# Kernel tuning notes

Hardware: AMD Instinct MI355X
Metric: run time of the kernel (lower is better)

Reference implementation:

```python
import jax, jax.numpy as jnp
import numpy as np

N_NODES = 100000
N_EDGES = 1600000
VOCAB = 10000
HIDDEN = 128
EMB1 = 128
EMB2 = 128
L1 = 64
N_GRAPHS = 256


def setup_inputs() -> dict:
    key = jax.random.key(0)
    ks = jax.random.split(key, 16)
    inp = {
        "x": jax.random.randint(ks[0], (N_NODES,), 0, VOCAB, dtype=jnp.int32),
        "edge_index": jax.random.randint(ks[1], (2, N_EDGES), 0, N_NODES, dtype=jnp.int32),
        "edge_weight": jax.random.uniform(ks[2], (N_EDGES,), dtype=jnp.float32),
        "batch": jnp.sort(jax.random.randint(ks[3], (N_NODES,), 0, N_GRAPHS, dtype=jnp.int32)),
        # parameters
        "emb_w": jax.random.normal(ks[4], (VOCAB, HIDDEN), dtype=jnp.float32) * 0.5,
        "w1_rel": jax.random.normal(ks[5], (EMB1, HIDDEN), dtype=jnp.float32) * (HIDDEN ** -0.5),
        "b1_rel": jnp.zeros((EMB1,), dtype=jnp.float32),
        "w1_root": jax.random.normal(ks[6], (EMB1, HIDDEN), dtype=jnp.float32) * (HIDDEN ** -0.5),
        "w2_rel": jax.random.normal(ks[7], (EMB2, EMB1), dtype=jnp.float32) * (EMB1 ** -0.5),
        "b2_rel": jnp.zeros((EMB2,), dtype=jnp.float32),
        "w2_root": jax.random.normal(ks[8], (EMB2, EMB1), dtype=jnp.float32) * (EMB1 ** -0.5),
        "cls1_w": jax.random.normal(ks[9], (L1, EMB2), dtype=jnp.float32) * (EMB2 ** -0.5),
        "cls1_b": jnp.zeros((L1,), dtype=jnp.float32),
        "cls2_w": jax.random.normal(ks[10], (2, L1), dtype=jnp.float32) * (L1 ** -0.5),
        "cls2_b": jnp.zeros((2,), dtype=jnp.float32),
    }
    return inp


def _embedding_max_norm(emb_w, idx, max_norm=1.0):
    # torch Embedding(max_norm=1): looked-up rows are renormalized to norm <= 1
    rows = emb_w[idx]                                        # [N, H]
    norm = jnp.linalg.norm(rows, axis=-1, keepdims=True)
    scale = jnp.minimum(1.0, max_norm / (norm + 1e-7))
    return rows * scale


def _graph_conv(h, src, dst, ew, w_rel, b_rel, w_root):
    # PyG GraphConv: out = lin_rel(sum_{j->i} w_ji * x_j) + lin_root(x_i)
    msg = h[src] * ew[:, None]                               # [E, D] gather
    agg = jax.ops.segment_sum(msg, dst, num_segments=N_NODES)  # [N, D] scatter-add
    return agg @ w_rel.T + b_rel + h @ w_root.T


def reference(x, edge_index, edge_weight, batch, emb_w,
              w1_rel, b1_rel, w1_root, w2_rel, b2_rel, w2_root,
              cls1_w, cls1_b, cls2_w, cls2_b):
    src, dst = edge_index[0], edge_index[1]
    h = _embedding_max_norm(emb_w, x)                        # [N, HIDDEN]
    # dropout is identity in eval mode
    h = jax.nn.relu(_graph_conv(h, src, dst, edge_weight, w1_rel, b1_rel, w1_root))
    h = jax.nn.relu(_graph_conv(h, src, dst, edge_weight, w2_rel, b2_rel, w2_root))
    # global mean pool over graphs
    sums = jax.ops.segment_sum(h, batch, num_segments=N_GRAPHS)        # [G, EMB2]
    counts = jax.ops.segment_sum(jnp.ones((h.shape[0],), h.dtype), batch,
                                 num_segments=N_GRAPHS)
    pooled = sums / jnp.maximum(counts, 1.0)[:, None]
    z = jax.nn.relu(pooled @ cls1_w.T + cls1_b)
    z = z @ cls2_w.T + cls2_b
    return jax.nn.softmax(z, axis=1)                          # [G, 2]
```

## Files before the change

### kernel.cpp

```cpp
#include <hip/hip_runtime.h>
#include <stdint.h>

#define NN 100000
#define NE 1600000
#define NG 256
#define NB 391
#define CHUNK 4096
#define NCH 391
#define NGS 392

typedef __attribute__((ext_vector_type(8))) short bf16x8;
typedef __attribute__((ext_vector_type(4))) float f32x4;

__device__ inline uint32_t f2bf(float f){
    uint32_t u = __float_as_uint(f);
    return (u + 0x7FFFu + ((u >> 16) & 1u)) >> 16;
}
__device__ inline float bflo(uint32_t u){ return __uint_as_float(u << 16); }
__device__ inline float bfhi(uint32_t u){ return __uint_as_float(u & 0xFFFF0000u); }
__device__ inline float bf1(short s){ return __uint_as_float(((uint32_t)(uint16_t)s) << 16); }

__global__ __launch_bounds__(256) void k_pack(const float* __restrict__ w1rel, const float* __restrict__ w1root,
                                              const float* __restrict__ w2rel, const float* __restrict__ w2root,
                                              short* __restrict__ wf, int* __restrict__ bcnt){
    int id = blockIdx.x * 256 + threadIdx.x;
    if (id < NB) bcnt[id] = 0;
    int i = id & 7, lane = (id >> 3) & 63, ks = (id >> 9) & 3, j0 = (id >> 11) & 7, m = id >> 14;
    const float* W = (m == 0) ? w1rel : (m == 1) ? w1root : (m == 2) ? w2rel : w2root;
    int j = j0 * 16 + (lane & 15);
    int k = ks * 32 + (lane >> 4) * 8 + i;
    wf[id] = (short)f2bf(W[j * 128 + k]);
}

__global__ __launch_bounds__(256) void k_embed(const int* __restrict__ x,
                                               const float* __restrict__ emb,
                                               uint32_t* __restrict__ hout,
                                               const int* __restrict__ edst,
                                               int* __restrict__ bcnt,
                                               const int* __restrict__ batch,
                                               int* __restrict__ gstart){
    int bid = blockIdx.x;
    if (bid < NN / 4){
        int w = threadIdx.x >> 6, l = threadIdx.x & 63;
        int n = bid * 4 + w;
        int r = x[n];
        const float2* e2 = (const float2*)emb;
        float2 v = e2[(size_t)r * 64 + l];
        float ss = v.x * v.x + v.y * v.y;
        #pragma unroll
        for (int off = 32; off; off >>= 1) ss += __shfl_xor(ss, off, 64);
        float sc = fminf(1.f, 1.f / (sqrtf(ss) + 1e-7f));
        hout[(size_t)n * 64 + l] = f2bf(v.x * sc) | (f2bf(v.y * sc) << 16);
    } else if (bid < NN / 4 + NCH){
        __shared__ int lh[NB];
        int t = threadIdx.x;
        int c0 = (bid - NN / 4) * CHUNK;
        int cnt = min(CHUNK, NE - c0);
        lh[t] = 0;
        if (t + 256 < NB) lh[t + 256] = 0;
        __syncthreads();
        for (int i = t; i < cnt; i += 256) atomicAdd(&lh[edst[c0 + i] >> 8], 1);
        __syncthreads();
        if (lh[t]) atomicAdd(&bcnt[t], lh[t]);
        if (t + 256 < NB && lh[t + 256]) atomicAdd(&bcnt[t + 256], lh[t + 256]);
    } else {
        int i = (bid - NN / 4 - NCH) * 256 + threadIdx.x;
        if (i > NN) return;
        int bprev = (i == 0) ? -1 : batch[i - 1];
        int bcur  = (i == NN) ? NG : batch[i];
        for (int g = bprev + 1; g <= bcur; ++g) gstart[g] = i;
    }
}

__global__ __launch_bounds__(256) void k_bscan(const int* __restrict__ bcnt,
                                               int* __restrict__ bbase, int* __restrict__ bfill,
                                               int* __restrict__ ptrA){
    __shared__ int sc[512];
    int t = threadIdx.x;
    int v0 = (t < NB) ? bcnt[t] : 0;
    int v1 = (t + 256 < NB) ? bcnt[t + 256] : 0;
    sc[t] = v0; sc[t + 256] = v1;
    __syncthreads();
    for (int off = 1; off < 512; off <<= 1){
        int u0 = (t >= off) ? sc[t - off] : 0;
        int u1 = sc[t + 256 - off];
        __syncthreads();
        sc[t] += u0; sc[t + 256] += u1;
        __syncthreads();
    }
    if (t < NB){ bbase[t] = sc[t] - v0; bfill[t] = 0; }
    if (t + 256 < NB){ bbase[t + 256] = sc[t + 256] - v1; bfill[t + 256] = 0; }
    if (t == 0){ bbase[NB] = NE; ptrA[NN] = NE; }
}

__global__ __launch_bounds__(256) void k_bscatter(const int* __restrict__ esrc, const int* __restrict__ edst,
                                                  const float* __restrict__ ew,
                                                  const int* __restrict__ bbase, int* __restrict__ bfill,
                                                  uint2* __restrict__ cse2){
    __shared__ uint2 rec[CHUNK];
    __shared__ unsigned short slotb[CHUNK];
    __shared__ int hist[512], start[512], gbase[512], sc[512];
    int t = threadIdx.x;
    int c0 = blockIdx.x * CHUNK;
    int cnt = min(CHUNK, NE - c0);
    hist[t] = 0; hist[t + 256] = 0;
    __syncthreads();
    for (int i = t; i < cnt; i += 256) atomicAdd(&hist[edst[c0 + i] >> 8], 1);
    __syncthreads();
    int v0 = hist[t], v1 = hist[t + 256];
    sc[t] = v0; sc[t + 256] = v1;
    __syncthreads();
    for (int off = 1; off < 512; off <<= 1){
        int u0 = (t >= off) ? sc[t - off] : 0;
        int u1 = sc[t + 256 - off];
        __syncthreads();
        sc[t] += u0; sc[t + 256] += u1;
        __syncthreads();
    }
    start[t] = sc[t] - v0;
    start[t + 256] = sc[t + 256] - v1;
    if (t < NB && v0 > 0) gbase[t] = bbase[t] + atomicAdd(&bfill[t], v0);
    if (t + 256 < NB && v1 > 0) gbase[t + 256] = bbase[t + 256] + atomicAdd(&bfill[t + 256], v1);
    __syncthreads();
    hist[t] = 0; hist[t + 256] = 0;
    __syncthreads();
    for (int i = t; i < cnt; i += 256){
        int d = edst[c0 + i];
        int b = d >> 8;
        int slot = start[b] + atomicAdd(&hist[b], 1);
        rec[slot] = make_uint2((uint32_t)esrc[c0 + i] | ((uint32_t)(d & 255) << 20),
                               __float_as_uint(ew[c0 + i]));
        slotb[slot] = (unsigned short)b;
    }
    __syncthreads();
    for (int i = t; i < cnt; i += 256){
        int b = slotb[i];
        cse2[gbase[b] + (i - start[b])] = rec[i];
    }
}

__global__ __launch_bounds__(256) void k_bcsr(const uint2* __restrict__ cse2,
                                              const int* __restrict__ bbase,
                                              int* __restrict__ ptrA,
                                              uint2* __restrict__ cse){
    __shared__ int cnt[256], sc[256], st[256];
    int t = threadIdx.x;
    int b = blockIdx.x;
    int ebase = bbase[b], eend = bbase[b + 1];
    int nb = b << 8;
    cnt[t] = 0;
    __syncthreads();
    for (int i = ebase + t; i < eend; i += 256){
        atomicAdd(&cnt[cse2[i].x >> 20], 1);
    }
    __syncthreads();
    int v = cnt[t];
    sc[t] = v;
    __syncthreads();
    for (int off = 1; off < 256; off <<= 1){
        int u = (t >= off) ? sc[t - off] : 0;
        __syncthreads();
        sc[t] += u;
        __syncthreads();
    }
    st[t] = sc[t] - v;
    if (nb + t < NN) ptrA[nb + t] = ebase + st[t];
    cnt[t] = 0;
    __syncthreads();
    for (int i = ebase + t; i < eend; i += 256){
        uint2 r = cse2[i];
        int dr = r.x >> 20;
        int pos = st[dr] + atomicAdd(&cnt[dr], 1);
        cse[ebase + pos] = make_uint2((r.x & 0xFFFFFu) << 8, r.y);
    }
}

#define ACC8(vv, ww) \
    a0 += ww * bflo(vv.x); a1 += ww * bfhi(vv.x); \
    a2 += ww * bflo(vv.y); a3 += ww * bfhi(vv.y); \
    a4 += ww * bflo(vv.z); a5 += ww * bfhi(vv.z); \
    a6 += ww * bflo(vv.w); a7 += ww * bfhi(vv.w);

__global__ __launch_bounds__(256) void k_agg(const uint32_t* __restrict__ hin,
                                             uint32_t* __restrict__ aggo,
                                             const int* __restrict__ ptr,
                                             const uint2* __restrict__ cse){
    int w = threadIdx.x >> 6, l = threadIdx.x & 63;
    int q = l >> 4, c = l & 15;
    int n = blockIdx.x * 4 + w;
    int p0 = ptr[n], p1 = ptr[n + 1];
    const char* hb = (const char*)hin;
    uint32_t coff = (uint32_t)(c << 4);
    float a0 = 0, a1 = 0, a2 = 0, a3 = 0, a4 = 0, a5 = 0, a6 = 0, a7 = 0;
    int e = p0;
    for (; e + 16 <= p1; e += 16){
        uint2 r0 = cse[e + q], r1 = cse[e + 4 + q], r2 = cse[e + 8 + q], r3 = cse[e + 12 + q];
        uint4 v0 = *(const uint4*)(hb + (r0.x + coff));
        uint4 v1 = *(const uint4*)(hb + (r1.x + coff));
        uint4 v2 = *(const uint4*)(hb + (r2.x + coff));
        uint4 v3 = *(const uint4*)(hb + (r3.x + coff));
        float w0 = __uint_as_float(r0.y), w1 = __uint_as_float(r1.y);
        float w2 = __uint_as_float(r2.y), w3 = __uint_as_float(r3.y);
        ACC8(v0, w0); ACC8(v1, w1); ACC8(v2, w2); ACC8(v3, w3);
    }
    for (; e + 8 <= p1; e += 8){
        uint2 r0 = cse[e + q], r1 = cse[e + 4 + q];
        uint4 v0 = *(const uint4*)(hb + (r0.x + coff));
        uint4 v1 = *(const uint4*)(hb + (r1.x + coff));
        float w0 = __uint_as_float(r0.y), w1 = __uint_as_float(r1.y);
        ACC8(v0, w0); ACC8(v1, w1);
    }
    for (; e + 4 <= p1; e += 4){
        uint2 r0 = cse[e + q];
        uint4 v0 = *(const uint4*)(hb + (r0.x + coff));
        float w0 = __uint_as_float(r0.y);
        ACC8(v0, w0);
    }
    if (e < p1){
        int idx = e + q;
        int cidx = (idx < p1) ? idx : (p1 - 1);
        uint2 r0 = cse[cidx];
        uint4 v0 = *(const uint4*)(hb + (r0.x + coff));
        float w0 = (idx < p1) ? __uint_as_float(r0.y) : 0.f;
        ACC8(v0, w0);
    }
    a0 += __shfl_xor(a0, 16, 64); a0 += __shfl_xor(a0, 32, 64);
    a1 += __shfl_xor(a1, 16, 64); a1 += __shfl_xor(a1, 32, 64);
    a2 += __shfl_xor(a2, 16, 64); a2 += __shfl_xor(a2, 32, 64);
    a3 += __shfl_xor(a3, 16, 64); a3 += __shfl_xor(a3, 32, 64);
    a4 += __shfl_xor(a4, 16, 64); a4 += __shfl_xor(a4, 32, 64);
    a5 += __shfl_xor(a5, 16, 64); a5 += __shfl_xor(a5, 32, 64);
    a6 += __shfl_xor(a6, 16, 64); a6 += __shfl_xor(a6, 32, 64);
    a7 += __shfl_xor(a7, 16, 64); a7 += __shfl_xor(a7, 32, 64);
    if (q == 0){
        uint4 o;
        o.x = f2bf(a0) | (f2bf(a1) << 16);
        o.y = f2bf(a2) | (f2bf(a3) << 16);
        o.z = f2bf(a4) | (f2bf(a5) << 16);
        o.w = f2bf(a6) | (f2bf(a7) << 16);
        *(uint4*)((char*)aggo + (size_t)n * 256 + coff) = o;
    }
}

__global__ __launch_bounds__(256) void k_gemm(const short* __restrict__ hin,
                                              const short* __restrict__ agg,
                                              short* __restrict__ hout,
                                              const bf16x8* __restrict__ wrel,
                                              const bf16x8* __restrict__ wroot,
                                              const float* __restrict__ bias){
    int t = threadIdx.x, w = t >> 6, l = t & 63;
    int rbase = blockIdx.x * 128 + w * 32;
    int r0 = rbase + (l & 15);
    int rA0 = min(r0, NN - 1);
    int rA1 = min(r0 + 16, NN - 1);
    int kb = (l >> 4) * 8;

    bf16x8 aA[2][4], aH[2][4];
    const short* pa0 = agg + (size_t)rA0 * 128 + kb;
    const short* pa1 = agg + (size_t)rA1 * 128 + kb;
    const short* ph0 = hin + (size_t)rA0 * 128 + kb;
    const short* ph1 = hin + (size_t)rA1 * 128 + kb;
    #pragma unroll
    for (int ks = 0; ks < 4; ++ks){
        aA[0][ks] = *(const bf16x8*)(pa0 + ks * 32);
        aA[1][ks] = *(const bf16x8*)(pa1 + ks * 32);
        aH[0][ks] = *(const bf16x8*)(ph0 + ks * 32);
        aH[1][ks] = *(const bf16x8*)(ph1 + ks * 32);
    }

    for (int j0 = 0; j0 < 8; ++j0){
        f32x4 acc0 = {0.f, 0.f, 0.f, 0.f}, acc1 = {0.f, 0.f, 0.f, 0.f};
        #pragma unroll
        for (int ks = 0; ks < 4; ++ks){
            bf16x8 br = wrel [(j0 * 4 + ks) * 64 + l];
            bf16x8 bo = wroot[(j0 * 4 + ks) * 64 + l];
            acc0 = __builtin_amdgcn_mfma_f32_16x16x32_bf16(aA[0][ks], br, acc0, 0, 0, 0);
            acc0 = __builtin_amdgcn_mfma_f32_16x16x32_bf16(aH[0][ks], bo, acc0, 0, 0, 0);
            acc1 = __builtin_amdgcn_mfma_f32_16x16x32_bf16(aA[1][ks], br, acc1, 0, 0, 0);
            acc1 = __builtin_amdgcn_mfma_f32_16x16x32_bf16(aH[1][ks], bo, acc1, 0, 0, 0);
        }
        int col = j0 * 16 + (l & 15);
        float bv = bias[col];
        int rb = rbase + (l >> 4) * 4;
        #pragma unroll
        for (int r = 0; r < 4; ++r){
            int row = rb + r;
            if (row < NN){
                float v = fmaxf(acc0[r] + bv, 0.f);
                hout[(size_t)row * 128 + col] = (short)f2bf(v);
            }
            int row1 = rb + 16 + r;
            if (row1 < NN){
                float v = fmaxf(acc1[r] + bv, 0.f);
                hout[(size_t)row1 * 128 + col] = (short)f2bf(v);
            }
        }
    }
}

__global__ __launch_bounds__(128) void k_poolcls(const short* __restrict__ h,
                                                 const int* __restrict__ gstart,
                                                 const float* __restrict__ c1w, const float* __restrict__ c1b,
                                                 const float* __restrict__ c2w, const float* __restrict__ c2b,
                                                 float* __restrict__ out){
    __shared__ float pl[128];
    __shared__ float z[64];
    __shared__ float logits[2];
    int g = blockIdx.x, t = threadIdx.x;
    int s = gstart[g], e = gstart[g + 1];
    float a0 = 0, a1 = 0, a2 = 0, a3 = 0;
    int i = s;
    for (; i + 3 < e; i += 4){
        a0 += bf1(h[(size_t)i * 128 + t]);
        a1 += bf1(h[(size_t)(i + 1) * 128 + t]);
        a2 += bf1(h[(size_t)(i + 2) * 128 + t]);
        a3 += bf1(h[(size_t)(i + 3) * 128 + t]);
    }
    for (; i < e; ++i) a0 += bf1(h[(size_t)i * 128 + t]);
    float sum = (a0 + a1) + (a2 + a3);
    int cnt = e - s;
    pl[t] = sum / fmaxf((float)cnt, 1.f);
    __syncthreads();
    if (t < 64){
        float acc = c1b[t];
        #pragma unroll 4
        for (int k = 0; k < 128; ++k) acc += pl[k] * c1w[t * 128 + k];
        z[t] = fmaxf(acc, 0.f);
    }
    __syncthreads();
    if (t < 2){
        float a = c2b[t];
        for (int k = 0; k < 64; ++k) a += z[k] * c2w[t * 64 + k];
        logits[t] = a;
    }
    __syncthreads();
    if (t == 0){
        float m = fmaxf(logits[0], logits[1]);
        float e0 = expf(logits[0] - m), e1 = expf(logits[1] - m);
        float ss = e0 + e1;
        out[g * 2 + 0] = e0 / ss;
        out[g * 2 + 1] = e1 / ss;
    }
}

extern "C" void kernel_launch(void* const* d_in, const int* in_sizes, int n_in,
                              void* d_out, int out_size, void* d_ws, size_t ws_size,
                              hipStream_t stream) {
    const int*   x      = (const int*)  d_in[0];
    const int*   eidx   = (const int*)  d_in[1];
    const float* ew     = (const float*)d_in[2];
    const int*   batch  = (const int*)  d_in[3];
    const float* emb    = (const float*)d_in[4];
    const float* w1rel  = (const float*)d_in[5];
    const float* b1     = (const float*)d_in[6];
    const float* w1root = (const float*)d_in[7];
    const float* w2rel  = (const float*)d_in[8];
    const float* b2     = (const float*)d_in[9];
    const float* w2root = (const float*)d_in[10];
    const float* c1w    = (const float*)d_in[11];
    const float* c1b    = (const float*)d_in[12];
    const float* c2w    = (const float*)d_in[13];
    const float* c2b    = (const float*)d_in[14];
    float* out = (float*)d_out;

    const int N = NN;
    const int E = NE;

    char* p = (char*)d_ws;
    auto alloc = [&](size_t bytes) -> void* {
        void* r = (void*)p;
        p += (bytes + 255) & ~(size_t)255;
        return r;
    };
    uint32_t* hA   = (uint32_t*)alloc((size_t)N * 64 * 4);
    uint32_t* hB   = (uint32_t*)alloc((size_t)N * 64 * 4);
    uint32_t* agg  = (uint32_t*)alloc((size_t)N * 64 * 4);
    int*   ptrA   = (int*)  alloc((size_t)(N + 1) * 4);
    int*   bcnt   = (int*)  alloc(NB * 4);
    int*   bbase  = (int*)  alloc((NB + 1) * 4);
    int*   bfill  = (int*)  alloc(NB * 4);
    uint2* cse2   = (uint2*)alloc((size_t)E * 8);
    uint2* cse    = (uint2*)alloc((size_t)E * 8);
    int*   gstart = (int*)  alloc((NG + 1) * 4);
    short* wf     = (short*)alloc(4 * 16384 * 2);
    (void)alloc(65536);

    const bf16x8* wf1rel  = (const bf16x8*)(wf);
    const bf16x8* wf1root = (const bf16x8*)(wf + 16384);
    const bf16x8* wf2rel  = (const bf16x8*)(wf + 32768);
    const bf16x8* wf2root = (const bf16x8*)(wf + 49152);

    const int* esrc = eidx;
    const int* edst = eidx + E;

    k_pack <<<256, 256, 0, stream>>>(w1rel, w1root, w2rel, w2root, wf, bcnt);
    k_embed<<<N / 4 + NCH + NGS, 256, 0, stream>>>(x, emb, hA, edst, bcnt, batch, gstart);

    k_bscan   <<<1,   256, 0, stream>>>(bcnt, bbase, bfill, ptrA);
    k_bscatter<<<NCH, 256, 0, stream>>>(esrc, edst, ew, bbase, bfill, cse2);
    k_bcsr    <<<NB,  256, 0, stream>>>(cse2, bbase, ptrA, cse);

    int ngemm = (N + 127) / 128;
    k_agg <<<N / 4, 256, 0, stream>>>(hA, agg, ptrA, cse);
    k_gemm<<<ngemm, 256, 0, stream>>>((const short*)hA, (const short*)agg, (short*)hB,
                                      wf1rel, wf1root, b1);
    k_agg <<<N / 4, 256, 0, stream>>>(hB, agg, ptrA, cse);
    k_gemm<<<ngemm, 256, 0, stream>>>((const short*)hB, (const short*)agg, (short*)hA,
                                      wf2rel, wf2root, b2);

    k_poolcls<<<NG, 128, 0, stream>>>((const short*)hA, gstart, c1w, c1b, c2w, c2b, out);
}
```

Measured before the change: 362.6 us.

## Fold weight packing and bucket scan into neighbors; shuffle-broadcast edge records in aggregation

Weight packing moves into the embed kernel as extra blocks, and the single-block bucket scan is recomputed redundantly inside every bscatter block. Counter zeroing becomes memsets. Together these cut two kernel launches and their serialization gaps. The aggregation kernel now loads 64 edge records per wave coalesced and broadcasts offsets and weights with shuffles instead of each quad reloading records. The cost is redundant scan work in each scatter block, plus shuffle overhead in the inner loop.

Measured after the change: 362.0 us. No clear change (-0.2%).

```diff
diff --git a/kernel.cpp b/kernel.cpp
--- a/kernel.cpp
+++ b/kernel.cpp
@@ -20,25 +20,16 @@
 __device__ inline float bfhi(uint32_t u){ return __uint_as_float(u & 0xFFFF0000u); }
 __device__ inline float bf1(short s){ return __uint_as_float(((uint32_t)(uint16_t)s) << 16); }
 
-__global__ __launch_bounds__(256) void k_pack(const float* __restrict__ w1rel, const float* __restrict__ w1root,
-                                              const float* __restrict__ w2rel, const float* __restrict__ w2root,
-                                              short* __restrict__ wf, int* __restrict__ bcnt){
-    int id = blockIdx.x * 256 + threadIdx.x;
-    if (id < NB) bcnt[id] = 0;
-    int i = id & 7, lane = (id >> 3) & 63, ks = (id >> 9) & 3, j0 = (id >> 11) & 7, m = id >> 14;
-    const float* W = (m == 0) ? w1rel : (m == 1) ? w1root : (m == 2) ? w2rel : w2root;
-    int j = j0 * 16 + (lane & 15);
-    int k = ks * 32 + (lane >> 4) * 8 + i;
-    wf[id] = (short)f2bf(W[j * 128 + k]);
-}
-
 __global__ __launch_bounds__(256) void k_embed(const int* __restrict__ x,
                                                const float* __restrict__ emb,
                                                uint32_t* __restrict__ hout,
                                                const int* __restrict__ edst,
                                                int* __restrict__ bcnt,
                                                const int* __restrict__ batch,
-                                               int* __restrict__ gstart){
+                                               int* __restrict__ gstart,
+                                               const float* __restrict__ w1rel, const float* __restrict__ w1root,
+                                               const float* __restrict__ w2rel, const float* __restrict__ w2root,
+                                               short* __restrict__ wf){
     int bid = blockIdx.x;
     if (bid < NN / 4){
         int w = threadIdx.x >> 6, l = threadIdx.x & 63;
@@ -63,23 +54,34 @@
         __syncthreads();
         if (lh[t]) atomicAdd(&bcnt[t], lh[t]);
         if (t + 256 < NB && lh[t + 256]) atomicAdd(&bcnt[t + 256], lh[t + 256]);
-    } else {
+    } else if (bid < NN / 4 + NCH + NGS){
         int i = (bid - NN / 4 - NCH) * 256 + threadIdx.x;
         if (i > NN) return;
         int bprev = (i == 0) ? -1 : batch[i - 1];
         int bcur  = (i == NN) ? NG : batch[i];
         for (int g = bprev + 1; g <= bcur; ++g) gstart[g] = i;
-    }
-}
-
-__global__ __launch_bounds__(256) void k_bscan(const int* __restrict__ bcnt,
-                                               int* __restrict__ bbase, int* __restrict__ bfill,
-                                               int* __restrict__ ptrA){
-    __shared__ int sc[512];
+    } else {
+        int id = (bid - NN / 4 - NCH - NGS) * 256 + threadIdx.x;
+        int i = id & 7, lane = (id >> 3) & 63, ks = (id >> 9) & 3, j0 = (id >> 11) & 7, m = id >> 14;
+        const float* W = (m == 0) ? w1rel : (m == 1) ? w1root : (m == 2) ? w2rel : w2root;
+        int j = j0 * 16 + (lane & 15);
+        int k = ks * 32 + (lane >> 4) * 8 + i;
+        wf[id] = (short)f2bf(W[j * 128 + k]);
+    }
+}
+
+__global__ __launch_bounds__(256) void k_bscatter(const int* __restrict__ esrc, const int* __restrict__ edst,
+                                                  const float* __restrict__ ew,
+                                                  const int* __restrict__ bcnt,
+                                                  int* __restrict__ bbase, int* __restrict__ bfill,
+                                                  uint2* __restrict__ cse2, int* __restrict__ ptrA){
+    __shared__ uint2 rec[CHUNK];
+    __shared__ unsigned short slotb[CHUNK];
+    __shared__ int bb[512], hist[512], start[512], gbase[512], sc[512];
     int t = threadIdx.x;
-    int v0 = (t < NB) ? bcnt[t] : 0;
-    int v1 = (t + 256 < NB) ? bcnt[t + 256] : 0;
-    sc[t] = v0; sc[t + 256] = v1;
+    int g0 = (t < NB) ? bcnt[t] : 0;
+    int g1 = (t + 256 < NB) ? bcnt[t + 256] : 0;
+    sc[t] = g0; sc[t + 256] = g1;
     __syncthreads();
     for (int off = 1; off < 512; off <<= 1){
         int u0 = (t >= off) ? sc[t - off] : 0;
@@ -88,23 +90,14 @@
         sc[t] += u0; sc[t + 256] += u1;
         __syncthreads();
     }
-    if (t < NB){ bbase[t] = sc[t] - v0; bfill[t] = 0; }
-    if (t + 256 < NB){ bbase[t + 256] = sc[t + 256] - v1; bfill[t + 256] = 0; }
+    bb[t] = sc[t] - g0; bb[t + 256] = sc[t + 256] - g1;
+    if (t < NB) bbase[t] = bb[t];
+    if (t + 256 < NB) bbase[t + 256] = bb[t + 256];
     if (t == 0){ bbase[NB] = NE; ptrA[NN] = NE; }
-}
-
-__global__ __launch_bounds__(256) void k_bscatter(const int* __restrict__ esrc, const int* __restrict__ edst,
-                                                  const float* __restrict__ ew,
-                                                  const int* __restrict__ bbase, int* __restrict__ bfill,
-                                                  uint2* __restrict__ cse2){
-    __shared__ uint2 rec[CHUNK];
-    __shared__ unsigned short slotb[CHUNK];
-    __shared__ int hist[512], start[512], gbase[512], sc[512];
-    int t = threadIdx.x;
+    hist[t] = 0; hist[t + 256] = 0;
+    __syncthreads();
     int c0 = blockIdx.x * CHUNK;
     int cnt = min(CHUNK, NE - c0);
-    hist[t] = 0; hist[t + 256] = 0;
-    __syncthreads();
     for (int i = t; i < cnt; i += 256) atomicAdd(&hist[edst[c0 + i] >> 8], 1);
     __syncthreads();
     int v0 = hist[t], v1 = hist[t + 256];
@@ -119,8 +112,8 @@
     }
     start[t] = sc[t] - v0;
     start[t + 256] = sc[t + 256] - v1;
-    if (t < NB && v0 > 0) gbase[t] = bbase[t] + atomicAdd(&bfill[t], v0);
-    if (t + 256 < NB && v1 > 0) gbase[t + 256] = bbase[t + 256] + atomicAdd(&bfill[t + 256], v1);
+    if (t < NB && v0 > 0) gbase[t] = bb[t] + atomicAdd(&bfill[t], v0);
+    if (t + 256 < NB && v1 > 0) gbase[t + 256] = bb[t + 256] + atomicAdd(&bfill[t + 256], v1);
     __syncthreads();
     hist[t] = 0; hist[t + 256] = 0;
     __syncthreads();
@@ -192,37 +185,30 @@
     const char* hb = (const char*)hin;
     uint32_t coff = (uint32_t)(c << 4);
     float a0 = 0, a1 = 0, a2 = 0, a3 = 0, a4 = 0, a5 = 0, a6 = 0, a7 = 0;
-    int e = p0;
-    for (; e + 16 <= p1; e += 16){
-        uint2 r0 = cse[e + q], r1 = cse[e + 4 + q], r2 = cse[e + 8 + q], r3 = cse[e + 12 + q];
-        uint4 v0 = *(const uint4*)(hb + (r0.x + coff));
-        uint4 v1 = *(const uint4*)(hb + (r1.x + coff));
-        uint4 v2 = *(const uint4*)(hb + (r2.x + coff));
-        uint4 v3 = *(const uint4*)(hb + (r3.x + coff));
-        float w0 = __uint_as_float(r0.y), w1 = __uint_as_float(r1.y);
-        float w2 = __uint_as_float(r2.y), w3 = __uint_as_float(r3.y);
-        ACC8(v0, w0); ACC8(v1, w1); ACC8(v2, w2); ACC8(v3, w3);
-    }
-    for (; e + 8 <= p1; e += 8){
-        uint2 r0 = cse[e + q], r1 = cse[e + 4 + q];
-        uint4 v0 = *(const uint4*)(hb + (r0.x + coff));
-        uint4 v1 = *(const uint4*)(hb + (r1.x + coff));
-        float w0 = __uint_as_float(r0.y), w1 = __uint_as_float(r1.y);
-        ACC8(v0, w0); ACC8(v1, w1);
-    }
-    for (; e + 4 <= p1; e += 4){
-        uint2 r0 = cse[e + q];
-        uint4 v0 = *(const uint4*)(hb + (r0.x + coff));
-        float w0 = __uint_as_float(r0.y);
-        ACC8(v0, w0);
-    }
-    if (e < p1){
-        int idx = e + q;
-        int cidx = (idx < p1) ? idx : (p1 - 1);
-        uint2 r0 = cse[cidx];
-        uint4 v0 = *(const uint4*)(hb + (r0.x + coff));
-        float w0 = (idx < p1) ? __uint_as_float(r0.y) : 0.f;
-        ACC8(v0, w0);
+    for (int base = p0; base < p1; base += 64){
+        int m = p1 - base; if (m > 64) m = 64;
+        int li = (l < m) ? l : (m - 1);
+        uint2 rec = cse[base + li];
+        int   myo = (int)rec.x;
+        float myw = (l < m) ? __uint_as_float(rec.y) : 0.f;
+        int e = 0;
+        for (; e + 16 <= m; e += 16){
+            int   o0 = __shfl(myo, e + q, 64);      float w0 = __shfl(myw, e + q, 64);
+            int   o1 = __shfl(myo, e + 4 + q, 64);  float w1 = __shfl(myw, e + 4 + q, 64);
+            int   o2 = __shfl(myo, e + 8 + q, 64);  float w2 = __shfl(myw, e + 8 + q, 64);
+            int   o3 = __shfl(myo, e + 12 + q, 64); float w3 = __shfl(myw, e + 12 + q, 64);
+            uint4 v0 = *(const uint4*)(hb + ((uint32_t)o0 + coff));
+            uint4 v1 = *(const uint4*)(hb + ((uint32_t)o1 + coff));
+            uint4 v2 = *(const uint4*)(hb + ((uint32_t)o2 + coff));
+            uint4 v3 = *(const uint4*)(hb + ((uint32_t)o3 + coff));
+            ACC8(v0, w0); ACC8(v1, w1); ACC8(v2, w2); ACC8(v3, w3);
+        }
+        for (; e < m; e += 4){
+            int   o0 = __shfl(myo, e + q, 64);
+            float w0 = __shfl(myw, e + q, 64);
+            uint4 v0 = *(const uint4*)(hb + ((uint32_t)o0 + coff));
+            ACC8(v0, w0);
+        }
     }
     a0 += __shfl_xor(a0, 16, 64); a0 += __shfl_xor(a0, 32, 64);
     a1 += __shfl_xor(a1, 16, 64); a1 += __shfl_xor(a1, 32, 64);
@@ -393,11 +379,13 @@
     const int* esrc = eidx;
     const int* edst = eidx + E;
 
-    k_pack <<<256, 256, 0, stream>>>(w1rel, w1root, w2rel, w2root, wf, bcnt);
-    k_embed<<<N / 4 + NCH + NGS, 256, 0, stream>>>(x, emb, hA, edst, bcnt, batch, gstart);
-
-    k_bscan   <<<1,   256, 0, stream>>>(bcnt, bbase, bfill, ptrA);
-    k_bscatter<<<NCH, 256, 0, stream>>>(esrc, edst, ew, bbase, bfill, cse2);
+    hipMemsetAsync(bcnt,  0, NB * 4, stream);
+    hipMemsetAsync(bfill, 0, NB * 4, stream);
+
+    k_embed<<<N / 4 + NCH + NGS + 256, 256, 0, stream>>>(x, emb, hA, edst, bcnt, batch, gstart,
+                                                         w1rel, w1root, w2rel, w2root, wf);
+
+    k_bscatter<<<NCH, 256, 0, stream>>>(esrc, edst, ew, bcnt, bbase, bfill, cse2, ptrA);
     k_bcsr    <<<NB,  256, 0, stream>>>(cse2, bbase, ptrA, cse);
 
     int ngemm = (N + 127) / 128;
```
